# Kernel optimization log

Measured on AMD Instinct MI355X. Metric: run time of the kernel, lower is better.

## Reference

```python
import jax, jax.numpy as jnp
import numpy as np
from jax import lax

B, T, E, H, ENC, NUM_LAYERS = 256, 100, 300, 512, 1024, 3
FORGET_BIAS = 1.0  # BasicLSTMCell default


def lstm_scan(x, W, b):
    """BasicLSTMCell over time. x: [B,T,E], W: [E+H,4H], b: [4H] -> hs: [B,T,H]."""
    def step(carry, xt):
        c, h = carry
        z = jnp.concatenate([xt, h], axis=-1) @ W + b  # [B,4H]
        i, j, f, o = jnp.split(z, 4, axis=-1)  # TF gate order i, j, f, o
        c = c * jax.nn.sigmoid(f + FORGET_BIAS) + jax.nn.sigmoid(i) * jnp.tanh(j)
        h = jnp.tanh(c) * jax.nn.sigmoid(o)
        return (c, h), h
    init = (jnp.zeros((x.shape[0], W.shape[1] // 4), x.dtype),) * 2
    _, hs = lax.scan(step, init, jnp.swapaxes(x, 0, 1))  # scan over T
    return jnp.swapaxes(hs, 0, 1)  # [B,T,H]


def last_output(hs, lengths):
    # reverse_sequence + slice[:, 0, :] == output at step length-1
    return hs[jnp.arange(hs.shape[0]), lengths - 1]  # [B,H]


def setup_inputs() -> dict:
    key = jax.random.key(0)
    ks = jax.random.split(key, 10)
    scale = 0.01  # random_normal_initializer(stddev=1/100)
    return {
        "left_embed": jax.random.normal(ks[0], (B, T, E), jnp.float32),
        "left_lengths": jax.random.randint(ks[1], (B,), 1, T + 1, jnp.int32),
        "right_embed": jax.random.normal(ks[2], (B, T, E), jnp.float32),
        "right_lengths": jax.random.randint(ks[3], (B,), 1, T + 1, jnp.int32),
        "W_left": jax.random.normal(ks[4], (E + H, 4 * H), jnp.float32) / np.sqrt(E + H),
        "b_left": jnp.zeros((4 * H,), jnp.float32),
        "W_right": jax.random.normal(ks[5], (E + H, 4 * H), jnp.float32) / np.sqrt(E + H),
        "b_right": jnp.zeros((4 * H,), jnp.float32),
        "trans_weights": scale * jax.random.normal(ks[6], (2 * H, ENC), jnp.float32),
        "hidden_weights": scale * jax.random.normal(ks[7], (NUM_LAYERS - 1, ENC, ENC), jnp.float32),
    }


def reference(left_embed, left_lengths, right_embed, right_lengths,
              W_left, b_left, W_right, b_right, trans_weights, hidden_weights):
    l_last = last_output(lstm_scan(left_embed, W_left, b_left), left_lengths)
    r_last = last_output(lstm_scan(right_embed, W_right, b_right), right_lengths)
    ctx = jnp.concatenate([l_last, r_last], axis=1)  # [B, 2H]
    x = jax.nn.relu(ctx @ trans_weights)
    for i in range(hidden_weights.shape[0]):  # dropout keep_prob=1.0 -> identity
        x = jax.nn.relu(x @ hidden_weights[i])
    return x  # [B, ENC]
```

## Files before the change

kernel.cpp:

```cpp
#include <hip/hip_runtime.h>
#include <math.h>

#define EDIM 300
#define HDIM 512
#define TDIM 100
#define BDIM 256
#define KTOT 812
#define KP   832
#define KHALF 416
#define NIT  13
#define ENC  1024
#define NBLK 256

#define B_C     0u
#define B_HHI   1048576u
#define B_HLO   2097152u
#define B_WPF   3145728u
#define B_CTX   9961472u
#define B_X1    11010048u
#define B_X2    12058624u
#define B_TWH   13107200u
#define B_TWL   19398656u
#define B_XSHI  25690112u
#define B_XSLO  56410112u

#define LW 0
#define LA(dbuf,half,hl) (107520 + (((((dbuf)*2)+(half))*2+(hl)) * 5120))
#define LRED 107520

typedef __attribute__((ext_vector_type(8))) short bf16x8;
typedef _Float16 f16x8 __attribute__((ext_vector_type(8)));
typedef __attribute__((ext_vector_type(4))) float f32x4;

__device__ __forceinline__ float fast_sigmoid(float x) {
    return 1.0f / (1.0f + __expf(-x));
}
__device__ __forceinline__ float fast_tanh(float x) {
    float t = __expf(2.0f * x);
    return 1.0f - 2.0f / (t + 1.0f);
}
__device__ __forceinline__ unsigned short bf16_rne(float v) {
    unsigned int u = __float_as_uint(v);
    unsigned int r = (u + 0x7fffu + ((u >> 16) & 1u)) >> 16;
    return (unsigned short)r;
}
__device__ __forceinline__ float bf16_to_f(unsigned short h) {
    return __uint_as_float(((unsigned int)h) << 16);
}
__device__ __forceinline__ void split2(float v, unsigned short& hi, unsigned short& lo) {
    hi = bf16_rne(v);
    lo = bf16_rne(v - bf16_to_f(hi));
}
__device__ __forceinline__ unsigned short f16_bits(float v) {
    _Float16 h = (_Float16)v;
    return *(unsigned short*)&h;
}
__device__ __forceinline__ float f16_val(unsigned short u) {
    _Float16 h = *(_Float16*)&u;
    return (float)h;
}
__device__ __forceinline__ void split_f16(float v, unsigned short& hi, unsigned short& lo) {
    hi = f16_bits(v);
    lo = f16_bits(v - f16_val(hi));
}

__global__ void zero_kernel(float* __restrict__ p, int n) {
    int i = blockIdx.x * blockDim.x + threadIdx.x;
    if (i < n) p[i] = 0.0f;
}

__global__ __launch_bounds__(256) void prep_w_lstm(
    const float* __restrict__ WL, const float* __restrict__ WR, char* __restrict__ ws)
{
    __shared__ float tile[64 * 65];
    int bid = blockIdx.x;
    int d = bid / (13 * 32);
    int rem = bid - d * (13 * 32);
    int kt = rem >> 5;
    int ct = rem & 31;
    const int k0 = kt * 64;
    const float* W = d ? WR : WL;
    for (int pass = 0; pass < 16; ++pass) {
        int idx = pass * 256 + threadIdx.x;
        int kk = idx >> 6, c = idx & 63;
        int g = c >> 4, hl = c & 15;
        int col = g * HDIM + ct * 16 + hl;
        int kg = k0 + kk;
        tile[kk * 65 + c] = (kg < KTOT) ? W[(size_t)kg * 2048 + col] : 0.0f;
    }
    __syncthreads();
    unsigned short* wf = (unsigned short*)(ws + B_WPF) + (size_t)d * 2048 * KP;
    for (int pass = 0; pass < 16; ++pass) {
        int idx = pass * 256 + threadIdx.x;
        int c = idx >> 6, kk = idx & 63;
        wf[(size_t)(ct * 64 + c) * KP + k0 + kk] = f16_bits(tile[kk * 65 + c]);
    }
}

__global__ __launch_bounds__(256) void prep_w_tail(
    const float* __restrict__ TW, const float* __restrict__ HW, char* __restrict__ ws)
{
    __shared__ float tile[64 * 65];
    int bid = blockIdx.x;
    int l = bid / 256;
    int rem = bid - l * 256;
    int kt = rem >> 4, ct = rem & 15;
    const int k0 = kt * 64, n0 = ct * 64;
    const float* W = (l == 0) ? TW : (HW + (size_t)(l - 1) * ENC * ENC);
    for (int pass = 0; pass < 16; ++pass) {
        int idx = pass * 256 + threadIdx.x;
        int kk = idx >> 6, c = idx & 63;
        tile[kk * 65 + c] = W[(size_t)(k0 + kk) * ENC + n0 + c];
    }
    __syncthreads();
    unsigned short* wh = (unsigned short*)(ws + B_TWH) + (size_t)l * ENC * ENC;
    unsigned short* wl = (unsigned short*)(ws + B_TWL) + (size_t)l * ENC * ENC;
    for (int pass = 0; pass < 16; ++pass) {
        int idx = pass * 256 + threadIdx.x;
        int c = idx >> 6, kk = idx & 63;
        unsigned short hi, lo;
        split2(tile[kk * 65 + c], hi, lo);
        size_t o = (size_t)(n0 + c) * ENC + k0 + kk;
        wh[o] = hi;
        wl[o] = lo;
    }
}

__global__ __launch_bounds__(256) void prep_x(
    const float* __restrict__ xL, const float* __restrict__ xR, char* __restrict__ ws)
{
    const long long NQ = 2LL * BDIM * TDIM * EDIM / 4;
    const long long N1 = (long long)BDIM * TDIM * EDIM;
    unsigned short* xh = (unsigned short*)(ws + B_XSHI);
    unsigned short* xl = (unsigned short*)(ws + B_XSLO);
    for (long long qi = blockIdx.x * blockDim.x + threadIdx.x; qi < NQ;
         qi += (long long)gridDim.x * blockDim.x) {
        long long i = qi * 4;
        const float* src = (i < N1) ? (xL + i) : (xR + (i - N1));
        float4 v = *(const float4*)src;
        ushort4 vh, vl;
        split_f16(v.x, vh.x, vl.x);
        split_f16(v.y, vh.y, vl.y);
        split_f16(v.z, vh.z, vl.z);
        split_f16(v.w, vh.w, vl.w);
        *(ushort4*)(xh + i) = vh;
        *(ushort4*)(xl + i) = vl;
    }
}

struct APack { ushort4 h0h, h0l, h1h, h1l; };

__global__ __launch_bounds__(512, 1) void lstm_step_f16(
    const int* __restrict__ lenL, const int* __restrict__ lenR,
    const float* __restrict__ bL, const float* __restrict__ bR,
    char* __restrict__ ws, int t, int par)
{
    __shared__ __align__(16) char smem[148480];

    const int bid   = blockIdx.x;
    const int ntile = (bid & 7) * 4 + ((bid >> 3) & 3);
    const int mt    = bid >> 5;
    const int n0    = ntile * 64;
    const int d     = mt >> 2;
    const int brow  = (mt & 3) * 64;

    const int* __restrict__ len    = d ? lenR : lenL;
    const float* __restrict__ bias = d ? bR : bL;

    float* __restrict__ cbuf = (float*)(ws + B_C);
    const unsigned short* __restrict__ hh_prev = (const unsigned short*)(ws + B_HHI) + (size_t)par * 262144;
    const unsigned short* __restrict__ hl_prev = (const unsigned short*)(ws + B_HLO) + (size_t)par * 262144;
    unsigned short* __restrict__ hh_next = (unsigned short*)(ws + B_HHI) + (size_t)(par ^ 1) * 262144;
    unsigned short* __restrict__ hl_next = (unsigned short*)(ws + B_HLO) + (size_t)(par ^ 1) * 262144;
    const unsigned short* __restrict__ Wp  = (const unsigned short*)(ws + B_WPF) + (size_t)d * 2048 * KP;
    const unsigned short* __restrict__ xsh = (const unsigned short*)(ws + B_XSHI);
    const unsigned short* __restrict__ xsl = (const unsigned short*)(ws + B_XSLO);
    float* __restrict__ ctx = (float*)(ws + B_CTX);

    const int tid  = threadIdx.x;
    const int l    = tid & 63;
    const int w    = tid >> 6;
    const int kh   = w >> 2;
    const int ms   = w & 3;
    const int fr   = l & 15;
    const int fg   = l >> 4;
    const int arow = tid >> 3;
    const int q    = (tid & 7) * 4;

    const int hcol = ntile * 16 + fr;
    const int row0 = brow + ms * 16 + fg * 4;
    const float bi  = bias[0 * HDIM + hcol];
    const float bj  = bias[1 * HDIM + hcol];
    const float bf_ = bias[2 * HDIM + hcol];
    const float bo  = bias[3 * HDIM + hcol];
    const int4 len4 = *(const int4*)(len + row0);
    float c_arr[4];
    {
        const size_t cb = (size_t)(d * BDIM + row0) * HDIM + hcol;
        c_arr[0] = cbuf[cb];
        c_arr[1] = cbuf[cb + HDIM];
        c_arr[2] = cbuf[cb + 2 * HDIM];
        c_arr[3] = cbuf[cb + 3 * HDIM];
    }

    {
        const unsigned short* src = Wp + (size_t)n0 * KP;
        #pragma unroll
        for (int i = 0; i < 26; ++i) {
            int idx = i * 512 + tid;
            int col = idx / 208;
            int kq  = (idx - col * 208) * 4;
            *(ushort4*)(smem + LW + (col * 840 + kq) * 2) =
                *(const ushort4*)(src + (size_t)col * KP + kq);
        }
    }

    const int grow = d * BDIM + brow + arow;

    auto ldA = [&](int it, APack& p) {
        #pragma unroll
        for (int hf = 0; hf < 2; ++hf) {
            const int kg = hf * KHALF + it * 32 + q;
            ushort4 vh, vl;
            if (kg < EDIM) {
                const size_t xo = ((size_t)grow * TDIM + t) * EDIM + kg;
                vh = *(const ushort4*)(xsh + xo);
                vl = *(const ushort4*)(xsl + xo);
            } else if (kg < KTOT) {
                const size_t hidx = (size_t)grow * HDIM + (kg - EDIM);
                vh = *(const ushort4*)(hh_prev + hidx);
                vl = *(const ushort4*)(hl_prev + hidx);
            } else {
                vh = make_ushort4(0, 0, 0, 0);
                vl = make_ushort4(0, 0, 0, 0);
            }
            if (hf == 0) { p.h0h = vh; p.h0l = vl; } else { p.h1h = vh; p.h1l = vl; }
        }
    };
    auto stA = [&](int dbuf, const APack& p) {
        const int o = (arow * 40 + q) * 2;
        *(ushort4*)(smem + LA(dbuf, 0, 0) + o) = p.h0h;
        *(ushort4*)(smem + LA(dbuf, 0, 1) + o) = p.h0l;
        *(ushort4*)(smem + LA(dbuf, 1, 0) + o) = p.h1h;
        *(ushort4*)(smem + LA(dbuf, 1, 1) + o) = p.h1l;
    };

    f32x4 acc[4] = {};
    APack pf[2];

    ldA(0, pf[0]);
    stA(0, pf[0]);
    ldA(1, pf[1]);

    #pragma unroll
    for (int it = 0; it < NIT; ++it) {
        if (it + 2 < NIT) ldA(it + 2, pf[it & 1]);
        __syncthreads();
        const int cur = it & 1;
        const int aoff = ((ms * 16 + fr) * 40 + fg * 8) * 2;
        const f16x8 ah = *(const f16x8*)(smem + LA(cur, kh, 0) + aoff);
        const f16x8 al = *(const f16x8*)(smem + LA(cur, kh, 1) + aoff);
        #pragma unroll
        for (int nf = 0; nf < 4; ++nf) {
            const f16x8 bv = *(const f16x8*)(smem + LW +
                ((nf * 16 + fr) * 840 + kh * KHALF + it * 32 + fg * 8) * 2);
            acc[nf] = __builtin_amdgcn_mfma_f32_16x16x32_f16(ah, bv, acc[nf], 0, 0, 0);
            acc[nf] = __builtin_amdgcn_mfma_f32_16x16x32_f16(al, bv, acc[nf], 0, 0, 0);
        }
        if (it + 1 < NIT) stA(cur ^ 1, pf[(it + 1) & 1]);
    }

    __syncthreads();
    float* red = (float*)(smem + LRED);
    if (kh == 1) {
        #pragma unroll
        for (int nf = 0; nf < 4; ++nf)
            #pragma unroll
            for (int r = 0; r < 4; ++r)
                red[(ms * 16 + fg * 4 + r) * 65 + nf * 16 + fr] = acc[nf][r];
    }
    __syncthreads();
    if (kh == 0) {
        #pragma unroll
        for (int nf = 0; nf < 4; ++nf)
            #pragma unroll
            for (int r = 0; r < 4; ++r)
                acc[nf][r] += red[(ms * 16 + fg * 4 + r) * 65 + nf * 16 + fr];

        const int lens[4] = { len4.x, len4.y, len4.z, len4.w };
        #pragma unroll
        for (int r = 0; r < 4; ++r) {
            const int row = row0 + r;
            const float iv = acc[0][r] + bi;
            const float jv = acc[1][r] + bj;
            const float fv = acc[2][r] + bf_;
            const float ov = acc[3][r] + bo;
            const float c_new = c_arr[r] * fast_sigmoid(fv + 1.0f)
                              + fast_sigmoid(iv) * fast_tanh(jv);
            const float h_new = fast_tanh(c_new) * fast_sigmoid(ov);
            const size_t hidx = (size_t)(d * BDIM + row) * HDIM + hcol;
            cbuf[hidx] = c_new;
            unsigned short hh, hl2;
            split_f16(h_new, hh, hl2);
            hh_next[hidx] = hh;
            hl_next[hidx] = hl2;
            if (t == lens[r] - 1) {
                ctx[(size_t)row * (2 * HDIM) + d * HDIM + hcol] = h_new;
            }
        }
    }
}

#define TL_AS_HI(hf) ((hf) * 5120)
#define TL_AS_LO(hf) (10240 + (hf) * 5120)
#define TL_BS_HI(hf) (20480 + (hf) * 5120)
#define TL_BS_LO(hf) (30720 + (hf) * 5120)

__global__ __launch_bounds__(512, 2) void gemm_relu_mfma(
    const float* __restrict__ A, const unsigned short* __restrict__ Wh,
    const unsigned short* __restrict__ Wl, float* __restrict__ C)
{
    const int ntile = blockIdx.x & 15;
    const int mt    = blockIdx.x >> 4;
    const int n0    = ntile * 64;
    const int m0    = mt * 64;

    __shared__ __align__(16) char smem[40960];

    const int tid  = threadIdx.x;
    const int l    = tid & 63;
    const int w    = tid >> 6;
    const int kh   = w >> 2;
    const int ms   = w & 3;
    const int fr   = l & 15;
    const int fg   = l >> 4;
    const int arow = tid >> 3;
    const int q    = (tid & 7) * 4;

    f32x4 acc[4] = {};

    for (int it = 0; it < 16; ++it) {
        #pragma unroll
        for (int hf = 0; hf < 2; ++hf) {
            const int kg = hf * 512 + it * 32 + q;
            const float4 v = *(const float4*)(A + (size_t)(m0 + arow) * ENC + kg);
            ushort4 vh, vl;
            split2(v.x, vh.x, vl.x);
            split2(v.y, vh.y, vl.y);
            split2(v.z, vh.z, vl.z);
            split2(v.w, vh.w, vl.w);
            *(ushort4*)(smem + TL_AS_HI(hf) + (arow * 40 + q) * 2) = vh;
            *(ushort4*)(smem + TL_AS_LO(hf) + (arow * 40 + q) * 2) = vl;
            const size_t wo = (size_t)(n0 + arow) * ENC + kg;
            *(ushort4*)(smem + TL_BS_HI(hf) + (arow * 40 + q) * 2) = *(const ushort4*)(Wh + wo);
            *(ushort4*)(smem + TL_BS_LO(hf) + (arow * 40 + q) * 2) = *(const ushort4*)(Wl + wo);
        }
        __syncthreads();
        const int aoff = ((ms * 16 + fr) * 40 + fg * 8) * 2;
        const bf16x8 ah = *(const bf16x8*)(smem + TL_AS_HI(kh) + aoff);
        const bf16x8 al = *(const bf16x8*)(smem + TL_AS_LO(kh) + aoff);
        #pragma unroll
        for (int nf = 0; nf < 4; ++nf) {
            const int boff = ((nf * 16 + fr) * 40 + fg * 8) * 2;
            const bf16x8 bh = *(const bf16x8*)(smem + TL_BS_HI(kh) + boff);
            const bf16x8 bl = *(const bf16x8*)(smem + TL_BS_LO(kh) + boff);
            acc[nf] = __builtin_amdgcn_mfma_f32_16x16x32_bf16(ah, bh, acc[nf], 0, 0, 0);
            acc[nf] = __builtin_amdgcn_mfma_f32_16x16x32_bf16(ah, bl, acc[nf], 0, 0, 0);
            acc[nf] = __builtin_amdgcn_mfma_f32_16x16x32_bf16(al, bh, acc[nf], 0, 0, 0);
        }
        __syncthreads();
    }

    float* red = (float*)smem;
    if (kh == 1) {
        #pragma unroll
        for (int nf = 0; nf < 4; ++nf)
            #pragma unroll
            for (int r = 0; r < 4; ++r)
                red[(ms * 16 + fg * 4 + r) * 65 + nf * 16 + fr] = acc[nf][r];
    }
    __syncthreads();
    if (kh == 0) {
        #pragma unroll
        for (int nf = 0; nf < 4; ++nf) {
            #pragma unroll
            for (int r = 0; r < 4; ++r) {
                float v = acc[nf][r] + red[(ms * 16 + fg * 4 + r) * 65 + nf * 16 + fr];
                v = v > 0.f ? v : 0.f;
                const int row = m0 + ms * 16 + fg * 4 + r;
                C[(size_t)row * ENC + n0 + nf * 16 + fr] = v;
            }
        }
    }
}

extern "C" void kernel_launch(void* const* d_in, const int* in_sizes, int n_in,
                              void* d_out, int out_size, void* d_ws, size_t ws_size,
                              hipStream_t stream) {
    const float* xL   = (const float*)d_in[0];
    const int*   lenL = (const int*)  d_in[1];
    const float* xR   = (const float*)d_in[2];
    const int*   lenR = (const int*)  d_in[3];
    const float* WL   = (const float*)d_in[4];
    const float* bL   = (const float*)d_in[5];
    const float* WR   = (const float*)d_in[6];
    const float* bR   = (const float*)d_in[7];
    const float* TW   = (const float*)d_in[8];
    const float* HW   = (const float*)d_in[9];
    char* ws   = (char*)d_ws;
    float* out = (float*)d_out;

    zero_kernel<<<3072, 256, 0, stream>>>((float*)ws, 786432);
    prep_w_lstm<<<832, 256, 0, stream>>>(WL, WR, ws);
    prep_w_tail<<<768, 256, 0, stream>>>(TW, HW, ws);
    prep_x<<<2048, 256, 0, stream>>>(xL, xR, ws);

    for (int t = 0; t < TDIM; ++t) {
        lstm_step_f16<<<NBLK, 512, 0, stream>>>(lenL, lenR, bL, bR, ws, t, t & 1);
    }

    float* ctx = (float*)(ws + B_CTX);
    float* x1  = (float*)(ws + B_X1);
    float* x2  = (float*)(ws + B_X2);
    const unsigned short* twh = (const unsigned short*)(ws + B_TWH);
    const unsigned short* twl = (const unsigned short*)(ws + B_TWL);
    gemm_relu_mfma<<<64, 512, 0, stream>>>(ctx, twh,                twl,                x1);
    gemm_relu_mfma<<<64, 512, 0, stream>>>(x1,  twh + 1024 * 1024, twl + 1024 * 1024,  x2);
    gemm_relu_mfma<<<64, 512, 0, stream>>>(x2,  twh + 2048 * 1024, twl + 2048 * 1024,  out);
}
```

Measured before the change: 1.260 ms.

## Hoist input projection out of LSTM recurrence into one batched GEMM

Computes x@Wx + bias for all timesteps up front in a single large MFMA GEMM kernel (prep_zx), stored as f16. The per-step kernel then only multiplies h by Wh (K=512 instead of 812), reads the precomputed gate contribution, and loads A fragments straight from global instead of staging them through LDS. This removes the per-step x load/split and shrinks the per-step weight staging, which cuts the serial recurrence cost. The trade-off is that the precomputed input term is rounded to f16, which may reduce accuracy, and a large zx buffer must be written and read.

```diff
diff --git a/kernel.cpp b/kernel.cpp
--- a/kernel.cpp
+++ b/kernel.cpp
@@ -6,30 +6,24 @@
 #define TDIM 100
 #define BDIM 256
 #define KTOT 812
-#define KP   832
-#define KHALF 416
-#define NIT  13
 #define ENC  1024
 #define NBLK 256
 
 #define B_C     0u
 #define B_HHI   1048576u
 #define B_HLO   2097152u
-#define B_WPF   3145728u
+#define B_WXF   3145728u
+#define B_WHF   5767168u
 #define B_CTX   9961472u
 #define B_X1    11010048u
 #define B_X2    12058624u
 #define B_TWH   13107200u
 #define B_TWL   19398656u
-#define B_XSHI  25690112u
-#define B_XSLO  56410112u
-
-#define LW 0
-#define LA(dbuf,half,hl) (107520 + (((((dbuf)*2)+(half))*2+(hl)) * 5120))
-#define LRED 107520
+#define B_ZX    25690112u
 
 typedef __attribute__((ext_vector_type(8))) short bf16x8;
 typedef _Float16 f16x8 __attribute__((ext_vector_type(8)));
+typedef __attribute__((ext_vector_type(8))) unsigned short u16x8;
 typedef __attribute__((ext_vector_type(4))) float f32x4;
 
 __device__ __forceinline__ float fast_sigmoid(float x) {
@@ -89,11 +83,16 @@
         tile[kk * 65 + c] = (kg < KTOT) ? W[(size_t)kg * 2048 + col] : 0.0f;
     }
     __syncthreads();
-    unsigned short* wf = (unsigned short*)(ws + B_WPF) + (size_t)d * 2048 * KP;
+    unsigned short* wx = (unsigned short*)(ws + B_WXF) + (size_t)d * 2048 * 320;
+    unsigned short* wh = (unsigned short*)(ws + B_WHF) + (size_t)d * 2048 * 512;
     for (int pass = 0; pass < 16; ++pass) {
         int idx = pass * 256 + threadIdx.x;
         int c = idx >> 6, kk = idx & 63;
-        wf[(size_t)(ct * 64 + c) * KP + k0 + kk] = f16_bits(tile[kk * 65 + c]);
+        int kg = k0 + kk;
+        unsigned short hv = f16_bits(tile[kk * 65 + c]);
+        int cp = ct * 64 + c;
+        if (kg < 320) wx[(size_t)cp * 320 + kg] = (kg < 300) ? hv : (unsigned short)0;
+        if (kg >= 300 && kg < KTOT) wh[(size_t)cp * 512 + (kg - 300)] = hv;
     }
 }
 
@@ -126,36 +125,102 @@
     }
 }
 
-__global__ __launch_bounds__(256) void prep_x(
-    const float* __restrict__ xL, const float* __restrict__ xR, char* __restrict__ ws)
+__global__ __launch_bounds__(512, 1) void prep_zx(
+    const float* __restrict__ xL, const float* __restrict__ xR,
+    const float* __restrict__ bL, const float* __restrict__ bR,
+    char* __restrict__ ws)
 {
-    const long long NQ = 2LL * BDIM * TDIM * EDIM / 4;
-    const long long N1 = (long long)BDIM * TDIM * EDIM;
-    unsigned short* xh = (unsigned short*)(ws + B_XSHI);
-    unsigned short* xl = (unsigned short*)(ws + B_XSLO);
-    for (long long qi = blockIdx.x * blockDim.x + threadIdx.x; qi < NQ;
-         qi += (long long)gridDim.x * blockDim.x) {
-        long long i = qi * 4;
-        const float* src = (i < N1) ? (xL + i) : (xR + (i - N1));
-        float4 v = *(const float4*)src;
-        ushort4 vh, vl;
-        split_f16(v.x, vh.x, vl.x);
-        split_f16(v.y, vh.y, vl.y);
-        split_f16(v.z, vh.z, vl.z);
-        split_f16(v.w, vh.w, vl.w);
-        *(ushort4*)(xh + i) = vh;
-        *(ushort4*)(xl + i) = vl;
-    }
-}
-
-struct APack { ushort4 h0h, h0l, h1h, h1l; };
-
-__global__ __launch_bounds__(512, 1) void lstm_step_f16(
+    __shared__ __align__(16) char smem[81920];
+    const int ntile = blockIdx.x;
+    const int m0    = blockIdx.y * 64;
+    const int d     = blockIdx.z;
+    const int n0    = ntile * 128;
+    const float* __restrict__ x    = d ? xR : xL;
+    const float* __restrict__ bias = d ? bR : bL;
+    const unsigned short* __restrict__ Wxp = (const unsigned short*)(ws + B_WXF) + (size_t)d * 2048 * 320;
+    unsigned short* __restrict__ zx = (unsigned short*)(ws + B_ZX) + (size_t)d * 25600 * 2048;
+
+    const int tid = threadIdx.x;
+    const int l   = tid & 63;
+    const int w   = tid >> 6;
+    const int kh  = w >> 2;
+    const int ms  = w & 3;
+    const int fr  = l & 15;
+    const int fg  = l >> 4;
+
+    #pragma unroll
+    for (int j = 0; j < 10; ++j) {
+        int c = j * 512 + tid;
+        int frag = c >> 6, ls = c & 63;
+        int khf = (frag >= 40) ? 1 : 0;
+        int f2 = frag - khf * 40;
+        int itf = f2 >> 3, nff = f2 & 7;
+        int colp = n0 + nff * 16 + (ls & 15);
+        int kk = khf * 160 + itf * 32 + (ls >> 4) * 8;
+        *(uint4*)(smem + frag * 1024 + ls * 16) =
+            *(const uint4*)(Wxp + (size_t)colp * 320 + kk);
+    }
+    __syncthreads();
+
+    f32x4 acc[8] = {};
+    const int rowX = m0 + ms * 16 + fr;
+    const float* __restrict__ xrow = x + (size_t)rowX * EDIM;
+    const int kb = kh * 160 + fg * 8;
+
+    #pragma unroll
+    for (int it = 0; it < 5; ++it) {
+        const int kg = kb + it * 32;
+        float4 f4a = (kg + 4 <= EDIM) ? *(const float4*)(xrow + kg) : make_float4(0.f, 0.f, 0.f, 0.f);
+        float4 f4b = (kg + 8 <= EDIM) ? *(const float4*)(xrow + kg + 4) : make_float4(0.f, 0.f, 0.f, 0.f);
+        u16x8 ahu, alu;
+        float vv[8] = { f4a.x, f4a.y, f4a.z, f4a.w, f4b.x, f4b.y, f4b.z, f4b.w };
+        #pragma unroll
+        for (int i = 0; i < 8; ++i) {
+            unsigned short hi, lo;
+            split_f16(vv[i], hi, lo);
+            ahu[i] = hi;
+            alu[i] = lo;
+        }
+        const f16x8 ah = *(f16x8*)&ahu;
+        const f16x8 al = *(f16x8*)&alu;
+        #pragma unroll
+        for (int nf = 0; nf < 8; ++nf) {
+            const f16x8 bv = *(const f16x8*)(smem + ((kh * 40 + it * 8 + nf) << 10) + l * 16);
+            acc[nf] = __builtin_amdgcn_mfma_f32_16x16x32_f16(ah, bv, acc[nf], 0, 0, 0);
+            acc[nf] = __builtin_amdgcn_mfma_f32_16x16x32_f16(al, bv, acc[nf], 0, 0, 0);
+        }
+    }
+
+    __syncthreads();
+    float* red = (float*)smem;
+    if (kh == 1) {
+        #pragma unroll
+        for (int nf = 0; nf < 8; ++nf)
+            #pragma unroll
+            for (int r = 0; r < 4; ++r)
+                red[(ms * 16 + fg * 4 + r) * 132 + nf * 16 + fr] = acc[nf][r];
+    }
+    __syncthreads();
+    if (kh == 0) {
+        #pragma unroll
+        for (int nf = 0; nf < 8; ++nf) {
+            const int col = (nf & 3) * HDIM + (ntile * 2 + (nf >> 2)) * 16 + fr;
+            const float bv = bias[col];
+            #pragma unroll
+            for (int r = 0; r < 4; ++r) {
+                const int rm = m0 + ms * 16 + fg * 4 + r;
+                float v = acc[nf][r] + red[(ms * 16 + fg * 4 + r) * 132 + nf * 16 + fr] + bv;
+                zx[(size_t)rm * 2048 + n0 + nf * 16 + fr] = f16_bits(v);
+            }
+        }
+    }
+}
+
+__global__ __launch_bounds__(512, 1) void lstm_step_h(
     const int* __restrict__ lenL, const int* __restrict__ lenR,
-    const float* __restrict__ bL, const float* __restrict__ bR,
     char* __restrict__ ws, int t, int par)
 {
-    __shared__ __align__(16) char smem[148480];
+    __shared__ __align__(16) char smem[65536];
 
     const int bid   = blockIdx.x;
     const int ntile = (bid & 7) * 4 + ((bid >> 3) & 3);
@@ -164,114 +229,82 @@
     const int d     = mt >> 2;
     const int brow  = (mt & 3) * 64;
 
-    const int* __restrict__ len    = d ? lenR : lenL;
-    const float* __restrict__ bias = d ? bR : bL;
+    const int* __restrict__ len = d ? lenR : lenL;
 
     float* __restrict__ cbuf = (float*)(ws + B_C);
     const unsigned short* __restrict__ hh_prev = (const unsigned short*)(ws + B_HHI) + (size_t)par * 262144;
     const unsigned short* __restrict__ hl_prev = (const unsigned short*)(ws + B_HLO) + (size_t)par * 262144;
     unsigned short* __restrict__ hh_next = (unsigned short*)(ws + B_HHI) + (size_t)(par ^ 1) * 262144;
     unsigned short* __restrict__ hl_next = (unsigned short*)(ws + B_HLO) + (size_t)(par ^ 1) * 262144;
-    const unsigned short* __restrict__ Wp  = (const unsigned short*)(ws + B_WPF) + (size_t)d * 2048 * KP;
-    const unsigned short* __restrict__ xsh = (const unsigned short*)(ws + B_XSHI);
-    const unsigned short* __restrict__ xsl = (const unsigned short*)(ws + B_XSLO);
+    const unsigned short* __restrict__ Whp = (const unsigned short*)(ws + B_WHF) + (size_t)d * 2048 * 512;
+    const unsigned short* __restrict__ zx  = (const unsigned short*)(ws + B_ZX) + (size_t)d * 25600 * 2048;
     float* __restrict__ ctx = (float*)(ws + B_CTX);
 
-    const int tid  = threadIdx.x;
-    const int l    = tid & 63;
-    const int w    = tid >> 6;
-    const int kh   = w >> 2;
-    const int ms   = w & 3;
-    const int fr   = l & 15;
-    const int fg   = l >> 4;
-    const int arow = tid >> 3;
-    const int q    = (tid & 7) * 4;
+    const int tid = threadIdx.x;
+    const int l   = tid & 63;
+    const int w   = tid >> 6;
+    const int kh  = w >> 2;
+    const int ms  = w & 3;
+    const int fr  = l & 15;
+    const int fg  = l >> 4;
 
     const int hcol = ntile * 16 + fr;
     const int row0 = brow + ms * 16 + fg * 4;
-    const float bi  = bias[0 * HDIM + hcol];
-    const float bj  = bias[1 * HDIM + hcol];
-    const float bf_ = bias[2 * HDIM + hcol];
-    const float bo  = bias[3 * HDIM + hcol];
     const int4 len4 = *(const int4*)(len + row0);
     float c_arr[4];
-    {
+    unsigned short zraw[16];
+    if (kh == 0) {
         const size_t cb = (size_t)(d * BDIM + row0) * HDIM + hcol;
         c_arr[0] = cbuf[cb];
         c_arr[1] = cbuf[cb + HDIM];
         c_arr[2] = cbuf[cb + 2 * HDIM];
         c_arr[3] = cbuf[cb + 3 * HDIM];
+        const size_t zb = ((size_t)row0 * TDIM + t) * 2048 + n0 + fr;
+        #pragma unroll
+        for (int r = 0; r < 4; ++r)
+            #pragma unroll
+            for (int nf = 0; nf < 4; ++nf)
+                zraw[r * 4 + nf] = zx[zb + (size_t)r * (TDIM * 2048) + nf * 16];
     }
 
     {
-        const unsigned short* src = Wp + (size_t)n0 * KP;
-        #pragma unroll
-        for (int i = 0; i < 26; ++i) {
-            int idx = i * 512 + tid;
-            int col = idx / 208;
-            int kq  = (idx - col * 208) * 4;
-            *(ushort4*)(smem + LW + (col * 840 + kq) * 2) =
-                *(const ushort4*)(src + (size_t)col * KP + kq);
-        }
-    }
-
-    const int grow = d * BDIM + brow + arow;
-
-    auto ldA = [&](int it, APack& p) {
-        #pragma unroll
-        for (int hf = 0; hf < 2; ++hf) {
-            const int kg = hf * KHALF + it * 32 + q;
-            ushort4 vh, vl;
-            if (kg < EDIM) {
-                const size_t xo = ((size_t)grow * TDIM + t) * EDIM + kg;
-                vh = *(const ushort4*)(xsh + xo);
-                vl = *(const ushort4*)(xsl + xo);
-            } else if (kg < KTOT) {
-                const size_t hidx = (size_t)grow * HDIM + (kg - EDIM);
-                vh = *(const ushort4*)(hh_prev + hidx);
-                vl = *(const ushort4*)(hl_prev + hidx);
-            } else {
-                vh = make_ushort4(0, 0, 0, 0);
-                vl = make_ushort4(0, 0, 0, 0);
-            }
-            if (hf == 0) { p.h0h = vh; p.h0l = vl; } else { p.h1h = vh; p.h1l = vl; }
-        }
-    };
-    auto stA = [&](int dbuf, const APack& p) {
-        const int o = (arow * 40 + q) * 2;
-        *(ushort4*)(smem + LA(dbuf, 0, 0) + o) = p.h0h;
-        *(ushort4*)(smem + LA(dbuf, 0, 1) + o) = p.h0l;
-        *(ushort4*)(smem + LA(dbuf, 1, 0) + o) = p.h1h;
-        *(ushort4*)(smem + LA(dbuf, 1, 1) + o) = p.h1l;
-    };
+        const unsigned short* __restrict__ Wsrc = Whp + (size_t)n0 * 512;
+        #pragma unroll
+        for (int j = 0; j < 8; ++j) {
+            int c = j * 512 + tid;
+            int frag = c >> 6, ls = c & 63;
+            int colp = (frag & 3) * 16 + (ls & 15);
+            int kk = (frag >> 5) * 256 + ((frag >> 2) & 7) * 32 + (ls >> 4) * 8;
+            *(uint4*)(smem + frag * 1024 + ls * 16) =
+                *(const uint4*)(Wsrc + (size_t)colp * 512 + kk);
+        }
+    }
+    __syncthreads();
 
     f32x4 acc[4] = {};
-    APack pf[2];
-
-    ldA(0, pf[0]);
-    stA(0, pf[0]);
-    ldA(1, pf[1]);
-
+    const size_t abase = (size_t)(d * BDIM + brow + ms * 16 + fr) * HDIM + kh * 256 + fg * 8;
+    uint4 ahc = *(const uint4*)(hh_prev + abase);
+    uint4 alc = *(const uint4*)(hl_prev + abase);
     #pragma unroll
-    for (int it = 0; it < NIT; ++it) {
-        if (it + 2 < NIT) ldA(it + 2, pf[it & 1]);
-        __syncthreads();
-        const int cur = it & 1;
-        const int aoff = ((ms * 16 + fr) * 40 + fg * 8) * 2;
-        const f16x8 ah = *(const f16x8*)(smem + LA(cur, kh, 0) + aoff);
-        const f16x8 al = *(const f16x8*)(smem + LA(cur, kh, 1) + aoff);
+    for (int it = 0; it < 8; ++it) {
+        uint4 ahn, aln;
+        if (it < 7) {
+            ahn = *(const uint4*)(hh_prev + abase + (it + 1) * 32);
+            aln = *(const uint4*)(hl_prev + abase + (it + 1) * 32);
+        }
+        const f16x8 ah = *(const f16x8*)&ahc;
+        const f16x8 al = *(const f16x8*)&alc;
         #pragma unroll
         for (int nf = 0; nf < 4; ++nf) {
-            const f16x8 bv = *(const f16x8*)(smem + LW +
-                ((nf * 16 + fr) * 840 + kh * KHALF + it * 32 + fg * 8) * 2);
+            const f16x8 bv = *(const f16x8*)(smem + ((kh * 32 + it * 4 + nf) << 10) + l * 16);
             acc[nf] = __builtin_amdgcn_mfma_f32_16x16x32_f16(ah, bv, acc[nf], 0, 0, 0);
             acc[nf] = __builtin_amdgcn_mfma_f32_16x16x32_f16(al, bv, acc[nf], 0, 0, 0);
         }
-        if (it + 1 < NIT) stA(cur ^ 1, pf[(it + 1) & 1]);
-    }
-
-    __syncthreads();
-    float* red = (float*)(smem + LRED);
+        if (it < 7) { ahc = ahn; alc = aln; }
+    }
+
+    __syncthreads();
+    float* red = (float*)smem;
     if (kh == 1) {
         #pragma unroll
         for (int nf = 0; nf < 4; ++nf)
@@ -281,20 +314,15 @@
     }
     __syncthreads();
     if (kh == 0) {
-        #pragma unroll
-        for (int nf = 0; nf < 4; ++nf)
-            #pragma unroll
-            for (int r = 0; r < 4; ++r)
-                acc[nf][r] += red[(ms * 16 + fg * 4 + r) * 65 + nf * 16 + fr];
-
         const int lens[4] = { len4.x, len4.y, len4.z, len4.w };
         #pragma unroll
         for (int r = 0; r < 4; ++r) {
             const int row = row0 + r;
-            const float iv = acc[0][r] + bi;
-            const float jv = acc[1][r] + bj;
-            const float fv = acc[2][r] + bf_;
-            const float ov = acc[3][r] + bo;
+            const int rb = (ms * 16 + fg * 4 + r) * 65;
+            const float iv = acc[0][r] + red[rb + 0 * 16 + fr] + f16_val(zraw[r * 4 + 0]);
+            const float jv = acc[1][r] + red[rb + 1 * 16 + fr] + f16_val(zraw[r * 4 + 1]);
+            const float fv = acc[2][r] + red[rb + 2 * 16 + fr] + f16_val(zraw[r * 4 + 2]);
+            const float ov = acc[3][r] + red[rb + 3 * 16 + fr] + f16_val(zraw[r * 4 + 3]);
             const float c_new = c_arr[r] * fast_sigmoid(fv + 1.0f)
                               + fast_sigmoid(iv) * fast_tanh(jv);
             const float h_new = fast_tanh(c_new) * fast_sigmoid(ov);
@@ -413,10 +441,10 @@
     zero_kernel<<<3072, 256, 0, stream>>>((float*)ws, 786432);
     prep_w_lstm<<<832, 256, 0, stream>>>(WL, WR, ws);
     prep_w_tail<<<768, 256, 0, stream>>>(TW, HW, ws);
-    prep_x<<<2048, 256, 0, stream>>>(xL, xR, ws);
+    prep_zx<<<dim3(16, 400, 2), 512, 0, stream>>>(xL, xR, bL, bR, ws);
 
     for (int t = 0; t < TDIM; ++t) {
-        lstm_step_f16<<<NBLK, 512, 0, stream>>>(lenL, lenR, bL, bR, ws, t, t & 1);
+        lstm_step_h<<<NBLK, 512, 0, stream>>>(lenL, lenR, ws, t, t & 1);
     }
 
     float* ctx = (float*)(ws + B_CTX);
```

Result: slower. 1.425 ms (+13.1%).
